# Performance work log

Hardware: AMD Instinct MI355X
Metric: run time of the kernel (lower is better)

The kernel has to match this reference:

```python
import jax, jax.numpy as jnp
import numpy as np

N_NODES = 100000
N_EDGES = 1600000
DIM_IN = 128
DIM_OUT = 128


def setup_inputs() -> dict:
    key = jax.random.key(0)
    k_x, k_e, k_w = jax.random.split(key, 3)
    x = jax.random.normal(k_x, (N_NODES, DIM_IN), dtype=jnp.float32)
    edge_index = jax.random.randint(k_e, (2, N_EDGES), 0, N_NODES, dtype=jnp.int64)
    # Glorot-uniform weight like PyG's GCNConv linear layer, stored [d_in, d_out]
    limit = np.sqrt(6.0 / (DIM_IN + DIM_OUT)).astype(np.float32)
    W = jax.random.uniform(k_w, (DIM_IN, DIM_OUT), dtype=jnp.float32, minval=-limit, maxval=limit)
    return {"x": x, "edge_index": edge_index, "W": W}


def reference(x, edge_index, W):
    # PyG GCNConv (bias=False): out = D^{-1/2} (A + I) D^{-1/2} (x @ W)
    N = x.shape[0]
    x_proj = x @ W  # [N, d_out]
    loop = jnp.arange(N, dtype=edge_index.dtype)
    src = jnp.concatenate([edge_index[0], loop])  # message sources (row)
    dst = jnp.concatenate([edge_index[1], loop])  # aggregation targets (col)
    # degree counted at target nodes (edge weight = 1), incl. self loops
    deg = jax.ops.segment_sum(jnp.ones(src.shape, dtype=x.dtype), dst, num_segments=N)
    dis = jnp.where(deg > 0, jax.lax.rsqrt(deg), 0.0)
    norm = dis[src] * dis[dst]  # [E+N]
    msgs = x_proj[src] * norm[:, None]  # [E+N, d_out] gather + scale
    return jax.ops.segment_sum(msgs, dst, num_segments=N)  # scatter-add
```

## Files before the change

kernel.cpp:

```cpp
#include <hip/hip_runtime.h>
#include <hip/hip_bf16.h>

#define DIM 128
#define PCH 4096

typedef __attribute__((ext_vector_type(8))) short bf16x8;
typedef __attribute__((ext_vector_type(4))) float f32x4;

__device__ __forceinline__ float bfu_lo(unsigned u) { return __uint_as_float(u << 16); }
__device__ __forceinline__ float bfu_hi(unsigned u) { return __uint_as_float(u & 0xffff0000u); }
__device__ __forceinline__ unsigned short f2bf(float f) {
    unsigned u = __float_as_uint(f);
    u += 0x7fffu + ((u >> 16) & 1u);
    return (unsigned short)(u >> 16);
}

__device__ __forceinline__ int edge_at(const void* ei, int idx64, long long pos) {
    return idx64 ? (int)__builtin_nontemporal_load((const long long*)ei + pos)
                 : __builtin_nontemporal_load((const int*)ei + pos);
}

__device__ __forceinline__ int detect_idx64(const void* ei, int E, unsigned* s_or, int* s_flag) {
    const unsigned* ei_w = (const unsigned*)ei;
    int t = threadIdx.x;
    unsigned o = 0;
    int lim = (E < 4096) ? E : 4096;
    for (int k = t; k < lim; k += 256) o |= ei_w[2 * k + 1];
    s_or[t] = o;
    __syncthreads();
    for (int s = 128; s > 0; s >>= 1) {
        if (t < s) s_or[t] |= s_or[t + s];
        __syncthreads();
    }
    if (t == 0) *s_flag = (s_or[0] == 0u) ? 1 : 0;
    __syncthreads();
    return *s_flag;
}

__global__ __launch_bounds__(256) void hist_detect(const void* ei, unsigned* bcnt,
                                                   int E, int shift) {
    __shared__ unsigned s_h[512];
    __shared__ unsigned s_or[256];
    __shared__ int s_flag;
    int t = threadIdx.x;
    for (int i = t; i < 512; i += 256) s_h[i] = 0u;
    int idx64 = detect_idx64(ei, E, s_or, &s_flag);
    long long stride = (long long)gridDim.x * 256;
    for (long long e = (long long)blockIdx.x * 256 + t; e < E; e += stride) {
        int d = edge_at(ei, idx64, (long long)E + e);
        atomicAdd(&s_h[d >> shift], 1u);
    }
    __syncthreads();
    for (int i = t; i < 512; i += 256)
        if (s_h[i]) atomicAdd(&bcnt[i], s_h[i]);
}

__global__ __launch_bounds__(256) void partition(const void* ei, const unsigned* __restrict__ bcnt,
                                                 unsigned* bcur0, long long* pout,
                                                 int E, int B, int shift) {
    __shared__ unsigned s_hist[512], s_off[512], s_gbase[512], s_pref[512], s_bbase[512];
    __shared__ unsigned wsum[4];
    __shared__ unsigned s_or[256];
    __shared__ int s_flag;
    __shared__ long long s_p[PCH];
    int t = threadIdx.x;
    long long base = (long long)blockIdx.x * PCH;
    for (int i = t; i < 512; i += 256) { s_hist[i] = 0u; s_off[i] = 0u; }
    int idx64 = detect_idx64(ei, E, s_or, &s_flag);

    {
        unsigned v0 = bcnt[2 * t], v1 = bcnt[2 * t + 1];
        unsigned ps = v0 + v1;
        unsigned s = ps;
        int lane = t & 63;
#pragma unroll
        for (int off = 1; off < 64; off <<= 1) {
            unsigned u = __shfl_up(s, off, 64);
            if (lane >= off) s += u;
        }
        int w = t >> 6;
        if (lane == 63) wsum[w] = s;
        __syncthreads();
        unsigned woff = 0;
        for (int j = 0; j < w; j++) woff += wsum[j];
        unsigned excl = woff + s - ps;
        s_bbase[2 * t] = excl;
        s_bbase[2 * t + 1] = excl + v0;
    }
    __syncthreads();

    int d_[PCH / 256], s_[PCH / 256];
#pragma unroll 4
    for (int j = 0; j < PCH / 256; j++) {
        long long e = base + j * 256 + t;
        if (e < E) {
            d_[j] = edge_at(ei, idx64, (long long)E + e);
            s_[j] = edge_at(ei, idx64, e);
            atomicAdd(&s_hist[d_[j] >> shift], 1u);
        } else d_[j] = -1;
    }
    __syncthreads();

    {
        unsigned v0 = s_hist[2 * t], v1 = s_hist[2 * t + 1];
        unsigned ps = v0 + v1;
        unsigned s = ps;
        int lane = t & 63;
#pragma unroll
        for (int off = 1; off < 64; off <<= 1) {
            unsigned u = __shfl_up(s, off, 64);
            if (lane >= off) s += u;
        }
        int w = t >> 6;
        if (lane == 63) wsum[w] = s;
        __syncthreads();
        unsigned woff = 0;
        for (int j = 0; j < w; j++) woff += wsum[j];
        unsigned excl = woff + s - ps;
        s_pref[2 * t] = excl;
        s_pref[2 * t + 1] = excl + v0;
    }
    __syncthreads();

    for (int i = t; i < B; i += 256)
        if (s_hist[i]) s_gbase[i] = s_bbase[i] + atomicAdd(&bcur0[i], s_hist[i]);
#pragma unroll 4
    for (int j = 0; j < PCH / 256; j++)
        if (d_[j] >= 0) {
            int b = d_[j] >> shift;
            unsigned p = s_pref[b] + atomicAdd(&s_off[b], 1u);
            s_p[p] = ((long long)s_[j] << 32) | (unsigned)d_[j];
        }
    __syncthreads();
    long long rem = (long long)E - base;
    unsigned tot = (rem < PCH) ? (unsigned)rem : (unsigned)PCH;
    for (unsigned i = t; i < tot; i += 256) {
        long long v = s_p[i];
        int b = ((int)v) >> shift;
        pout[s_gbase[b] + (i - s_pref[b])] = v;
    }
}

__global__ __launch_bounds__(256) void build_csr(const long long* __restrict__ pairs,
                                                 const unsigned* __restrict__ bcnt,
                                                 unsigned* deg, unsigned* row_start,
                                                 float* dis, int* col_src,
                                                 int N, int shift) {
    __shared__ unsigned cnt[512], cur[512], pref[512];
    __shared__ unsigned s_bb[513];
    __shared__ unsigned wsum[4];
    int b = blockIdx.x, t = threadIdx.x;
    int npb = 1 << shift;
    if (npb > 512) npb = 512;
    int nodeLo = b << shift;

    {
        unsigned v0 = bcnt[2 * t], v1 = bcnt[2 * t + 1];
        unsigned ps = v0 + v1;
        unsigned s = ps;
        int lane = t & 63;
#pragma unroll
        for (int off = 1; off < 64; off <<= 1) {
            unsigned u = __shfl_up(s, off, 64);
            if (lane >= off) s += u;
        }
        int w = t >> 6;
        if (lane == 63) wsum[w] = s;
        __syncthreads();
        unsigned woff = 0;
        for (int j = 0; j < w; j++) woff += wsum[j];
        unsigned excl = woff + s - ps;
        s_bb[2 * t] = excl;
        s_bb[2 * t + 1] = excl + v0;
        if (t == 255) s_bb[512] = excl + ps;
    }
    __syncthreads();
    unsigned lo = s_bb[b], hi = s_bb[b + 1];

    for (int i = t; i < npb; i += 256) cnt[i] = 0u;
    __syncthreads();
    for (unsigned e = lo + t; e < hi; e += 256) {
        int d = (int)pairs[e];
        atomicAdd(&cnt[d - nodeLo], 1u);
    }
    __syncthreads();
    unsigned v0 = (2 * t < npb) ? cnt[2 * t] : 0u;
    unsigned v1 = (2 * t + 1 < npb) ? cnt[2 * t + 1] : 0u;
    unsigned ps = v0 + v1;
    unsigned s = ps;
    int lane = t & 63;
#pragma unroll
    for (int off = 1; off < 64; off <<= 1) {
        unsigned u = __shfl_up(s, off, 64);
        if (lane >= off) s += u;
    }
    int w = t >> 6;
    if (lane == 63) wsum[w] = s;
    __syncthreads();
    unsigned woff = 0;
    for (int j = 0; j < w; j++) woff += wsum[j];
    unsigned excl = woff + s - ps;
    if (2 * t < npb) pref[2 * t] = excl;
    if (2 * t + 1 < npb) pref[2 * t + 1] = excl + v0;
    __syncthreads();
    for (int i = t; i < npb; i += 256) {
        int node = nodeLo + i;
        unsigned rs = lo + pref[i];
        if (node < N) {
            unsigned c = cnt[i];
            deg[node] = c;
            row_start[node] = rs;
            dis[node] = rsqrtf((float)c + 1.0f);
        }
        cur[i] = rs;
    }
    __syncthreads();
    for (unsigned e = lo + t; e < hi; e += 256) {
        long long v = pairs[e];
        int d = (int)v;
        int sv = (int)(v >> 32);
        unsigned pos = atomicAdd(&cur[d - nodeLo], 1u);
        col_src[pos] = sv;
    }
}

__global__ __launch_bounds__(256) void gemm_xw(const float* __restrict__ x,
                                               const float* __restrict__ W,
                                               const float* __restrict__ dis,
                                               unsigned short* __restrict__ xps, int N) {
    __shared__ unsigned short wt[128 * 136];
    int tid = threadIdx.x;
    for (int idx = tid; idx < DIM * DIM; idx += 256) {
        int k = idx >> 7, n = idx & 127;
        wt[n * 136 + k] = f2bf(W[idx]);
    }
    __syncthreads();

    int wv = tid >> 6, lane = tid & 63;
    int l15 = lane & 15, quad = lane >> 4;
    int rowBase = blockIdx.x * 128 + wv * 32;

    f32x4 acc[2][8];
#pragma unroll
    for (int mt = 0; mt < 2; mt++)
#pragma unroll
        for (int nt = 0; nt < 8; nt++)
            acc[mt][nt] = (f32x4){0.f, 0.f, 0.f, 0.f};

#pragma unroll
    for (int k0 = 0; k0 < DIM; k0 += 32) {
        bf16x8 aa[2], bb[8];
#pragma unroll
        for (int mt = 0; mt < 2; mt++) {
            int r = rowBase + mt * 16 + l15;
            if (r > N - 1) r = N - 1;
            const float* xf = x + (size_t)r * DIM + k0 + quad * 8;
            float4 u0 = ((const float4*)xf)[0];
            float4 u1 = ((const float4*)xf)[1];
            bf16x8 a;
            a[0] = (short)f2bf(u0.x); a[1] = (short)f2bf(u0.y);
            a[2] = (short)f2bf(u0.z); a[3] = (short)f2bf(u0.w);
            a[4] = (short)f2bf(u1.x); a[5] = (short)f2bf(u1.y);
            a[6] = (short)f2bf(u1.z); a[7] = (short)f2bf(u1.w);
            aa[mt] = a;
        }
#pragma unroll
        for (int nt = 0; nt < 8; nt++)
            bb[nt] = *(const bf16x8*)(wt + (nt * 16 + l15) * 136 + k0 + quad * 8);
#pragma unroll
        for (int mt = 0; mt < 2; mt++)
#pragma unroll
            for (int nt = 0; nt < 8; nt++)
                acc[mt][nt] = __builtin_amdgcn_mfma_f32_16x16x32_bf16(bb[nt], aa[mt], acc[mt][nt], 0, 0, 0);
    }

#pragma unroll
    for (int mt = 0; mt < 2; mt++) {
        int r = rowBase + mt * 16 + l15;
        if (r < N) {
            float sc = dis[r];
#pragma unroll
            for (int nt = 0; nt < 8; nt++) {
                int c0 = nt * 16 + quad * 4;
                ushort4 o;
                o.x = f2bf(acc[mt][nt][0] * sc);
                o.y = f2bf(acc[mt][nt][1] * sc);
                o.z = f2bf(acc[mt][nt][2] * sc);
                o.w = f2bf(acc[mt][nt][3] * sc);
                *(ushort4*)(xps + (size_t)r * DIM + c0) = o;
            }
        }
    }
}

__global__ __launch_bounds__(256) void aggregate(const unsigned short* __restrict__ xps,
                                                 const unsigned* __restrict__ row_start,
                                                 const unsigned* __restrict__ deg,
                                                 const float* __restrict__ dis,
                                                 const int* __restrict__ col_src,
                                                 float* __restrict__ out, int N) {
    int wid = (int)((blockIdx.x * 256 + threadIdx.x) >> 6);
    if (wid >= N) return;
    int lane = threadIdx.x & 63;
    int grp = lane >> 4, lin = lane & 15;
    const uint4* xp4 = (const uint4*)xps;

    float acc[8];
#pragma unroll
    for (int j = 0; j < 8; j++) acc[j] = 0.f;

    unsigned rs = row_start[wid];
    unsigned cnt = deg[wid];
    unsigned tot = cnt + 1;

    for (unsigned base = 0; base < tot; base += 64) {
        unsigned slot = base + (unsigned)lane;
        int idx = (slot < cnt) ? col_src[rs + slot] : wid;
        unsigned rem = tot - base; if (rem > 64) rem = 64;
        for (unsigned q = 0; q * 8 < rem; q++) {
            unsigned sl0 = q * 8 + (unsigned)grp;
            unsigned sl1 = sl0 + 4;
            int s0 = __shfl(idx, (int)sl0, 64);
            int s1 = __shfl(idx, (int)sl1, 64);
            float m0 = (sl0 < rem) ? 1.f : 0.f;
            float m1 = (sl1 < rem) ? 1.f : 0.f;
            uint4 v0 = xp4[(size_t)s0 * 16 + lin];
            uint4 v1 = xp4[(size_t)s1 * 16 + lin];
            acc[0] = fmaf(bfu_lo(v0.x), m0, acc[0]);
            acc[1] = fmaf(bfu_hi(v0.x), m0, acc[1]);
            acc[2] = fmaf(bfu_lo(v0.y), m0, acc[2]);
            acc[3] = fmaf(bfu_hi(v0.y), m0, acc[3]);
            acc[4] = fmaf(bfu_lo(v0.z), m0, acc[4]);
            acc[5] = fmaf(bfu_hi(v0.z), m0, acc[5]);
            acc[6] = fmaf(bfu_lo(v0.w), m0, acc[6]);
            acc[7] = fmaf(bfu_hi(v0.w), m0, acc[7]);
            acc[0] = fmaf(bfu_lo(v1.x), m1, acc[0]);
            acc[1] = fmaf(bfu_hi(v1.x), m1, acc[1]);
            acc[2] = fmaf(bfu_lo(v1.y), m1, acc[2]);
            acc[3] = fmaf(bfu_hi(v1.y), m1, acc[3]);
            acc[4] = fmaf(bfu_lo(v1.z), m1, acc[4]);
            acc[5] = fmaf(bfu_hi(v1.z), m1, acc[5]);
            acc[6] = fmaf(bfu_lo(v1.w), m1, acc[6]);
            acc[7] = fmaf(bfu_hi(v1.w), m1, acc[7]);
        }
    }

#pragma unroll
    for (int j = 0; j < 8; j++) {
        acc[j] += __shfl_xor(acc[j], 16, 64);
        acc[j] += __shfl_xor(acc[j], 32, 64);
    }

    float di = dis[wid];
    if (grp < 2) {
        int jb = (grp & 1) * 4;
        float4 o;
        o.x = acc[jb + 0] * di;
        o.y = acc[jb + 1] * di;
        o.z = acc[jb + 2] * di;
        o.w = acc[jb + 3] * di;
        *(float4*)(out + (size_t)wid * DIM + lin * 8 + jb) = o;
    }
}

extern "C" void kernel_launch(void* const* d_in, const int* in_sizes, int n_in,
                              void* d_out, int out_size, void* d_ws, size_t ws_size,
                              hipStream_t stream) {
    const int N = in_sizes[0] / DIM;
    const int E = in_sizes[1] / 2;
    const float* x = (const float*)d_in[0];
    const void* ei = d_in[1];
    const float* W = (const float*)d_in[2];
    float* out = (float*)d_out;

    int shift = 8;
    while ((((long long)N + (1LL << shift) - 1) >> shift) > 512 && shift < 9) shift++;
    int B = (int)(((long long)N + (1LL << shift) - 1) >> shift);

    char* wsp = (char*)d_ws;
    size_t off = 0;
    auto alloc = [&](size_t b) { void* p = wsp + off; off += (b + 255) & ~(size_t)255; return p; };
    unsigned* bcnt       = (unsigned*)alloc(4096);
    unsigned* bcur0      = bcnt + 512;
    unsigned* deg        = (unsigned*)alloc((size_t)N * 4);
    unsigned* row_start  = (unsigned*)alloc((size_t)N * 4);
    float*    dis        = (float*)alloc((size_t)N * 4);
    int*      col_src    = (int*)alloc((size_t)E * 4);
    unsigned short* xps  = (unsigned short*)alloc((size_t)N * DIM * 2);

    long long* pairs = (long long*)xps;
    if ((size_t)E * 8 > (size_t)N * DIM * 2 && off + (size_t)E * 8 <= ws_size)
        pairs = (long long*)alloc((size_t)E * 8);

    hipMemsetAsync(bcnt, 0, 4096, stream);
    hist_detect<<<512, 256, 0, stream>>>(ei, bcnt, E, shift);
    partition<<<(E + PCH - 1) / PCH, 256, 0, stream>>>(ei, bcnt, bcur0, pairs, E, B, shift);
    build_csr<<<B, 256, 0, stream>>>(pairs, bcnt, deg, row_start, dis, col_src, N, shift);
    gemm_xw<<<(N + 127) / 128, 256, 0, stream>>>(x, W, dis, xps, N);
    aggregate<<<(N + 3) / 4, 256, 0, stream>>>(xps, row_start, deg, dis, col_src, out, N);
}
```

Measured before the change: 243.8 us.

## Pack edge pairs into 32-bit words and reuse index-width flag across kernels

```diff
diff --git a/kernel.cpp b/kernel.cpp
--- a/kernel.cpp
+++ b/kernel.cpp
@@ -2,7 +2,7 @@
 #include <hip/hip_bf16.h>
 
 #define DIM 128
-#define PCH 4096
+#define PCH 2048
 
 typedef __attribute__((ext_vector_type(8))) short bf16x8;
 typedef __attribute__((ext_vector_type(4))) float f32x4;
@@ -38,13 +38,14 @@
 }
 
 __global__ __launch_bounds__(256) void hist_detect(const void* ei, unsigned* bcnt,
-                                                   int E, int shift) {
+                                                   int* flags, int E, int shift) {
     __shared__ unsigned s_h[512];
     __shared__ unsigned s_or[256];
     __shared__ int s_flag;
     int t = threadIdx.x;
     for (int i = t; i < 512; i += 256) s_h[i] = 0u;
     int idx64 = detect_idx64(ei, E, s_or, &s_flag);
+    if (blockIdx.x == 0 && t == 0) flags[0] = idx64;
     long long stride = (long long)gridDim.x * 256;
     for (long long e = (long long)blockIdx.x * 256 + t; e < E; e += stride) {
         int d = edge_at(ei, idx64, (long long)E + e);
@@ -55,18 +56,17 @@
         if (s_h[i]) atomicAdd(&bcnt[i], s_h[i]);
 }
 
-__global__ __launch_bounds__(256) void partition(const void* ei, const unsigned* __restrict__ bcnt,
-                                                 unsigned* bcur0, long long* pout,
+__global__ __launch_bounds__(256) void partition(const void* ei, const int* __restrict__ flags,
+                                                 const unsigned* __restrict__ bcnt,
+                                                 unsigned* bcur0, unsigned* pout,
                                                  int E, int B, int shift) {
     __shared__ unsigned s_hist[512], s_off[512], s_gbase[512], s_pref[512], s_bbase[512];
     __shared__ unsigned wsum[4];
-    __shared__ unsigned s_or[256];
-    __shared__ int s_flag;
-    __shared__ long long s_p[PCH];
+    __shared__ unsigned d_arr[PCH], s_arr[PCH];
     int t = threadIdx.x;
     long long base = (long long)blockIdx.x * PCH;
     for (int i = t; i < 512; i += 256) { s_hist[i] = 0u; s_off[i] = 0u; }
-    int idx64 = detect_idx64(ei, E, s_or, &s_flag);
+    int idx64 = flags[0];
 
     {
         unsigned v0 = bcnt[2 * t], v1 = bcnt[2 * t + 1];
@@ -90,7 +90,7 @@
     __syncthreads();
 
     int d_[PCH / 256], s_[PCH / 256];
-#pragma unroll 4
+#pragma unroll
     for (int j = 0; j < PCH / 256; j++) {
         long long e = base + j * 256 + t;
         if (e < E) {
@@ -124,24 +124,27 @@
 
     for (int i = t; i < B; i += 256)
         if (s_hist[i]) s_gbase[i] = s_bbase[i] + atomicAdd(&bcur0[i], s_hist[i]);
-#pragma unroll 4
+#pragma unroll
     for (int j = 0; j < PCH / 256; j++)
         if (d_[j] >= 0) {
             int b = d_[j] >> shift;
             unsigned p = s_pref[b] + atomicAdd(&s_off[b], 1u);
-            s_p[p] = ((long long)s_[j] << 32) | (unsigned)d_[j];
+            d_arr[p] = (unsigned)d_[j];
+            s_arr[p] = (unsigned)s_[j];
         }
     __syncthreads();
     long long rem = (long long)E - base;
     unsigned tot = (rem < PCH) ? (unsigned)rem : (unsigned)PCH;
+    unsigned msk = (1u << shift) - 1u;
     for (unsigned i = t; i < tot; i += 256) {
-        long long v = s_p[i];
-        int b = ((int)v) >> shift;
-        pout[s_gbase[b] + (i - s_pref[b])] = v;
-    }
-}
-
-__global__ __launch_bounds__(256) void build_csr(const long long* __restrict__ pairs,
+        unsigned d = d_arr[i];
+        int b = (int)(d >> shift);
+        unsigned packed = ((d & msk) << (32 - shift)) | s_arr[i];
+        pout[s_gbase[b] + (i - s_pref[b])] = packed;
+    }
+}
+
+__global__ __launch_bounds__(256) void build_csr(const unsigned* __restrict__ pairs,
                                                  const unsigned* __restrict__ bcnt,
                                                  unsigned* deg, unsigned* row_start,
                                                  float* dis, int* col_src,
@@ -153,6 +156,7 @@
     int npb = 1 << shift;
     if (npb > 512) npb = 512;
     int nodeLo = b << shift;
+    unsigned smask = (1u << (32 - shift)) - 1u;
 
     {
         unsigned v0 = bcnt[2 * t], v1 = bcnt[2 * t + 1];
@@ -180,8 +184,8 @@
     for (int i = t; i < npb; i += 256) cnt[i] = 0u;
     __syncthreads();
     for (unsigned e = lo + t; e < hi; e += 256) {
-        int d = (int)pairs[e];
-        atomicAdd(&cnt[d - nodeLo], 1u);
+        unsigned p = pairs[e];
+        atomicAdd(&cnt[p >> (32 - shift)], 1u);
     }
     __syncthreads();
     unsigned v0 = (2 * t < npb) ? cnt[2 * t] : 0u;
@@ -216,11 +220,10 @@
     }
     __syncthreads();
     for (unsigned e = lo + t; e < hi; e += 256) {
-        long long v = pairs[e];
-        int d = (int)v;
-        int sv = (int)(v >> 32);
-        unsigned pos = atomicAdd(&cur[d - nodeLo], 1u);
-        col_src[pos] = sv;
+        unsigned p = pairs[e];
+        unsigned dlow = p >> (32 - shift);
+        unsigned pos = atomicAdd(&cur[dlow], 1u);
+        col_src[pos] = (int)(p & smask);
     }
 }
 
@@ -382,19 +385,20 @@
     auto alloc = [&](size_t b) { void* p = wsp + off; off += (b + 255) & ~(size_t)255; return p; };
     unsigned* bcnt       = (unsigned*)alloc(4096);
     unsigned* bcur0      = bcnt + 512;
+    int*      flags      = (int*)alloc(256);
     unsigned* deg        = (unsigned*)alloc((size_t)N * 4);
     unsigned* row_start  = (unsigned*)alloc((size_t)N * 4);
     float*    dis        = (float*)alloc((size_t)N * 4);
     int*      col_src    = (int*)alloc((size_t)E * 4);
     unsigned short* xps  = (unsigned short*)alloc((size_t)N * DIM * 2);
 
-    long long* pairs = (long long*)xps;
-    if ((size_t)E * 8 > (size_t)N * DIM * 2 && off + (size_t)E * 8 <= ws_size)
-        pairs = (long long*)alloc((size_t)E * 8);
+    unsigned* pairs = (unsigned*)xps;
+    if ((size_t)E * 4 > (size_t)N * DIM * 2 && off + (size_t)E * 4 <= ws_size)
+        pairs = (unsigned*)alloc((size_t)E * 4);
 
     hipMemsetAsync(bcnt, 0, 4096, stream);
-    hist_detect<<<512, 256, 0, stream>>>(ei, bcnt, E, shift);
-    partition<<<(E + PCH - 1) / PCH, 256, 0, stream>>>(ei, bcnt, bcur0, pairs, E, B, shift);
+    hist_detect<<<512, 256, 0, stream>>>(ei, bcnt, flags, E, shift);
+    partition<<<(E + PCH - 1) / PCH, 256, 0, stream>>>(ei, flags, bcnt, bcur0, pairs, E, B, shift);
     build_csr<<<B, 256, 0, stream>>>(pairs, bcnt, deg, row_start, dis, col_src, N, shift);
     gemm_xw<<<(N + 127) / 128, 256, 0, stream>>>(x, W, dis, xps, N);
     aggregate<<<(N + 3) / 4, 256, 0, stream>>>(xps, row_start, deg, dis, col_src, out, N);
```

Result: no change. 244.9 us (+0.4%).
